# Kernel optimization log

Hardware: AMD Instinct MI355X
Metric: run time of the kernel (lower is better)

The kernel has to match this reference:

```python
import math
import jax, jax.numpy as jnp
import numpy as np

NUM_BUCKETS = 32
MAX_DISTANCE = 128
N_HEADS = 16
D_KV = 64


def relative_position_bucket(rel_pos, num_buckets=NUM_BUCKETS, max_distance=MAX_DISTANCE):
    # bidirectional=True path of the original
    n = -rel_pos
    nb = num_buckets // 2
    ret = (n < 0).astype(jnp.int32) * nb
    n = jnp.abs(n)
    max_exact = nb // 2
    is_small = n < max_exact
    val_large = max_exact + (
        jnp.log(n.astype(jnp.float32) / max_exact)
        / math.log(max_distance / max_exact)
        * (nb - max_exact)
    ).astype(jnp.int32)
    val_large = jnp.minimum(val_large, nb - 1)
    return jnp.where(is_small, n, val_large) + ret


def setup_inputs() -> dict:
    key = jax.random.key(0)
    ks = jax.random.split(key, 6)
    B, S, D = 2, 2048, 1024
    inner = N_HEADS * D_KV  # 1024
    sc = 1.0 / math.sqrt(D)
    return {
        "x": jax.random.normal(ks[0], (B, S, D), dtype=jnp.float32),
        "Wq": jax.random.normal(ks[1], (D, inner), dtype=jnp.float32) * sc,
        "Wk": jax.random.normal(ks[2], (D, inner), dtype=jnp.float32) * sc,
        "Wv": jax.random.normal(ks[3], (D, inner), dtype=jnp.float32) * sc,
        "Wo": jax.random.normal(ks[4], (inner, D), dtype=jnp.float32) * sc,
        "rel_table": jax.random.normal(ks[5], (NUM_BUCKETS, N_HEADS), dtype=jnp.float32),
        "attention_mask": jnp.zeros((B, 1, 1, S), dtype=jnp.float32),
    }


def reference(x, Wq, Wk, Wv, Wo, rel_table, attention_mask):
    B, S, D = x.shape
    H, Dk = N_HEADS, D_KV

    q = (x @ Wq).reshape(B, S, H, Dk).transpose(0, 2, 1, 3)  # bhqd
    k = (x @ Wk).reshape(B, S, H, Dk).transpose(0, 2, 1, 3)
    v = (x @ Wv).reshape(B, S, H, Dk).transpose(0, 2, 1, 3)

    # NOTE: T5 attention has no 1/sqrt(d) scaling
    scores = jnp.einsum('bhqd,bhkd->bhqk', q.astype(jnp.float32), k.astype(jnp.float32))

    pos = jnp.arange(S)
    rel_pos = pos[None, :] - pos[:, None]  # [S,S] = k_pos - q_pos
    buckets = relative_position_bucket(rel_pos)
    position_bias = jnp.transpose(rel_table[buckets], (2, 0, 1))  # [H,S,S]

    scores = scores + position_bias[None, ...] + attention_mask
    weights = jax.nn.softmax(scores, axis=-1)
    out = jnp.einsum('bhqk,bhkd->bhqd', weights, v.astype(jnp.float32))
    out = out.transpose(0, 2, 1, 3).reshape(B, S, H * Dk).astype(x.dtype)
    out = out @ Wo
    return (out, position_bias)
```

## Files before the change

kernel.cpp:

```cpp
#include <hip/hip_runtime.h>
#include <hip/hip_bf16.h>
#include <math.h>
#include <stdint.h>

typedef __bf16 bf16_t;
typedef __attribute__((ext_vector_type(8))) __bf16 bf16x8;
typedef __attribute__((ext_vector_type(4))) float f32x4;
typedef float f32x4a __attribute__((ext_vector_type(4), aligned(4)));
typedef unsigned short u16;
typedef unsigned int u32;

#define DEV static __device__ __forceinline__
#define LOG2E 1.4426950408889634f

DEV u16 f2b(float f){ bf16_t h = (bf16_t)f; return __builtin_bit_cast(u16, h); }
DEV float b2f(u16 u){ bf16_t h = __builtin_bit_cast(bf16_t, u); return (float)h; }
DEV f32x4 mfma16(bf16x8 a, bf16x8 b, f32x4 c){
  return __builtin_amdgcn_mfma_f32_16x16x32_bf16(a, b, c, 0, 0, 0);
}

#if __has_builtin(__builtin_amdgcn_exp2f)
DEV float fexp2(float x){ return __builtin_amdgcn_exp2f(x); }
#else
DEV float fexp2(float x){ return exp2f(x); }
#endif

DEV void gld16(const void* g, void* l){
  __builtin_amdgcn_global_load_lds((const __attribute__((address_space(1))) u32*)g,
                                   (__attribute__((address_space(3))) u32*)l, 16, 0, 0);
}

DEV bf16x8 ldsA64(const u16* arr, int row, int ch){
  return *(const bf16x8*)&arr[row*64 + ((ch ^ (row&7))*8)];
}
DEV bf16x8 ldsA32(const u16* arr, int row, int ch){
  return *(const bf16x8*)&arr[row*32 + ((ch ^ ((row>>1)&3))*8)];
}

__global__ __launch_bounds__(256) void k_prep(const float* __restrict__ x,
                                              const float* __restrict__ Wq, const float* __restrict__ Wk,
                                              const float* __restrict__ Wv, const float* __restrict__ Wo,
                                              const float* __restrict__ rel_table, const float* __restrict__ mask,
                                              u16* __restrict__ xh, u16* __restrict__ xl,
                                              u16* __restrict__ wth, u16* __restrict__ wot,
                                              float* __restrict__ bt, float* __restrict__ bt2,
                                              float* __restrict__ msk2){
  __shared__ float tile[64][65];
  int bid = blockIdx.x;
  int t = threadIdx.x;
  if(bid < 4096){
    size_t i = ((size_t)bid*256 + t)*4;
    float4 v = *(const float4*)(x + i);
    ushort4 hv, lv; float f, hf;
    f=v.x; hv.x=f2b(f); hf=b2f(hv.x); lv.x=f2b(f-hf);
    f=v.y; hv.y=f2b(f); hf=b2f(hv.y); lv.y=f2b(f-hf);
    f=v.z; hv.z=f2b(f); hf=b2f(hv.z); lv.z=f2b(f-hf);
    f=v.w; hv.w=f2b(f); hf=b2f(hv.w); lv.w=f2b(f-hf);
    *(ushort4*)(xh+i) = hv;
    *(ushort4*)(xl+i) = lv;
  } else if(bid < 5120){
    int rr = bid - 4096;
    int z = rr >> 8, ky = (rr >> 4) & 15, nx = rr & 15;
    const float* W = (z==0)?Wq:((z==1)?Wk:((z==2)?Wv:Wo));
    int n0 = nx*64, k0 = ky*64;
    int r = t>>6, c = t&63;
    #pragma unroll
    for(int i=0;i<16;i++){
      int row = i*4 + r;
      tile[row][c] = W[(size_t)(k0+row)*1024 + n0 + c];
    }
    __syncthreads();
    #pragma unroll
    for(int i=0;i<16;i++){
      int nrow = i*4 + r;
      float v = tile[c][nrow];
      size_t o = (size_t)(n0+nrow)*1024 + k0 + c;
      if(z<3) wth[(size_t)z*1048576 + o] = f2b(v);
      else    wot[o] = f2b(v);
    }
  } else {
    int gid = (bid-5120)*256 + t;
    if(gid < 4096) msk2[gid] = mask[gid]*LOG2E;
    int h = gid >> 12, idx = gid & 4095;
    float v = 0.f;
    if(idx < 4095){
      int delta = idx - 2047;
      int n = -delta;
      int ret = 0;
      if(n < 0){ ret = 16; n = -n; }
      int bucket;
      if(n < 8) bucket = n + ret;
      else {
        float a = (float)log((double)n * 0.125);
        float rr2 = (float)((double)a / (double)2.7725887298583984f);
        int vl = 8 + (int)(rr2 * 8.0f);
        vl = vl > 15 ? 15 : vl;
        bucket = vl + ret;
      }
      v = rel_table[bucket*16 + h];
    }
    bt[gid] = v;
    bt2[gid] = v*LOG2E - 32.0f;
  }
}

__global__ __launch_bounds__(256) void k_gemm_qkv(const u16* __restrict__ xh, const u16* __restrict__ xl,
                                                  const u16* __restrict__ wth,
                                                  u16* __restrict__ qh, u16* __restrict__ ql,
                                                  u16* __restrict__ kh, u16* __restrict__ vt){
  __shared__ __align__(16) u16 SM[24576];
  int z = blockIdx.z;
  const u16* WH = wth + (size_t)z*1048576;
  int lin2 = blockIdx.x + 8*blockIdx.y;
  int nl2 = (lin2 & 7)*32 + (lin2 >> 3);
  int n0 = (nl2 & 7)*128, m0 = (nl2 >> 3)*128;
  int t = threadIdx.x, w = t>>6, lane = t&63, l16 = lane&15, g = lane>>4;
  f32x4 acc[4][4];
  #pragma unroll
  for(int i=0;i<4;i++)
    #pragma unroll
    for(int j=0;j<4;j++) acc[i][j] = {0.f,0.f,0.f,0.f};
  int rbase = (w>>1)*64, cbase = (w&1)*64;

  #pragma unroll
  for(int jj=0;jj<6;jj++){
    int q = w + 4*jj;
    int arr = q>>3, sub = q&7;
    if(z!=0 && arr==1) continue;
    int row = sub*16 + (lane>>2);
    int lch = (lane&3) ^ ((row>>1)&3);
    const u16* src;
    if(arr==0)      src = xh + (size_t)(m0+row)*1024 + lch*8;
    else if(arr==1) src = xl + (size_t)(m0+row)*1024 + lch*8;
    else            src = WH + (size_t)(n0+row)*1024 + lch*8;
    gld16(src, &SM[q*512]);
  }
  __syncthreads();

  for(int it=0; it<32; ++it){
    const u16* Ah = SM + (it&1)*12288;
    const u16* Al = Ah + 4096;
    const u16* Bh = Ah + 8192;
    if(it < 31){
      u16* dstb = SM + ((it+1)&1)*12288;
      int kn = (it+1)*32;
      #pragma unroll
      for(int jj=0;jj<6;jj++){
        int q = w + 4*jj;
        int arr = q>>3, sub = q&7;
        if(z!=0 && arr==1) continue;
        int row = sub*16 + (lane>>2);
        int lch = (lane&3) ^ ((row>>1)&3);
        const u16* src;
        if(arr==0)      src = xh + (size_t)(m0+row)*1024 + kn + lch*8;
        else if(arr==1) src = xl + (size_t)(m0+row)*1024 + kn + lch*8;
        else            src = WH + (size_t)(n0+row)*1024 + kn + lch*8;
        gld16(src, dstb + q*512);
      }
      __builtin_amdgcn_sched_barrier(0);
    }
    if(z!=0){
      bf16x8 ah[4];
      #pragma unroll
      for(int i=0;i<4;i++) ah[i] = ldsA32(Ah, rbase + i*16 + l16, g);
      #pragma unroll
      for(int j=0;j<4;j++){
        bf16x8 bh = ldsA32(Bh, cbase + j*16 + l16, g);
        #pragma unroll
        for(int i=0;i<4;i++)
          acc[i][j] = mfma16(ah[i], bh, acc[i][j]);
      }
    } else {
      bf16x8 ah[4], am[4];
      #pragma unroll
      for(int i=0;i<4;i++){
        int row = rbase + i*16 + l16;
        ah[i] = ldsA32(Ah, row, g);
        am[i] = ldsA32(Al, row, g);
      }
      #pragma unroll
      for(int j=0;j<4;j++){
        bf16x8 bh = ldsA32(Bh, cbase + j*16 + l16, g);
        #pragma unroll
        for(int i=0;i<4;i++){
          acc[i][j] = mfma16(ah[i], bh, acc[i][j]);
          acc[i][j] = mfma16(am[i], bh, acc[i][j]);
        }
      }
    }
    __syncthreads();
  }
  if(z==2){
    #pragma unroll
    for(int i=0;i<4;i++)
      #pragma unroll
      for(int j=0;j<4;j++)
        #pragma unroll
        for(int r=0;r<4;r++){
          int ml = rbase + i*16 + g*4 + r;
          int nl = cbase + j*16 + l16;
          SM[nl*136 + ml] = f2b(acc[i][j][r]);
        }
    __syncthreads();
    int bb = m0 >> 11;
    #pragma unroll
    for(int kk=0;kk<8;kk++){
      int id = t + 256*kk;
      int row = id>>4, ch = id&15;
      uint4 v = *(const uint4*)&SM[row*136 + ch*8];
      int n = n0 + row;
      size_t dst = ((size_t)(bb*16 + (n>>6))*64 + (n&63))*2048 + (m0&2047) + ch*8;
      *(uint4*)&vt[dst] = v;
    }
  } else {
    #pragma unroll
    for(int i=0;i<4;i++)
      #pragma unroll
      for(int j=0;j<4;j++)
        #pragma unroll
        for(int r=0;r<4;r++){
          int m = m0 + rbase + i*16 + g*4 + r;
          int n = n0 + cbase + j*16 + l16;
          float v = acc[i][j][r];
          if(z==0) v *= LOG2E;
          int b = m >> 11, s = m & 2047;
          int hh = n >> 6, d = n & 63;
          size_t a = ((size_t)(b*16+hh)*2048 + s)*64 + d;
          u16 hb = f2b(v);
          if(z==0){ qh[a]=hb; ql[a]=f2b(v - b2f(hb)); }
          else    { kh[a]=hb; }
        }
  }
}

__global__ __launch_bounds__(256,4) void k_attn(const u16* __restrict__ qh, const u16* __restrict__ ql,
                                              const u16* __restrict__ kh,
                                              const u16* __restrict__ vt, const float* __restrict__ bt2,
                                              const float* __restrict__ msk2,
                                              const float* __restrict__ bt, float* __restrict__ bias_out,
                                              u16* __restrict__ ao){
  __shared__ __align__(16) u16 SM[20480];
  int lin = blockIdx.x + 32*blockIdx.y;
  int nlw = (lin & 7)*128 + (lin >> 3);
  int qx = nlw & 31, bh = nlw >> 5;
  int b = bh>>4, h = bh&15;
  int q0 = qx*64;
  int t = threadIdx.x, w = t>>6, lane = t&63, l16 = lane&15, g = lane>>4;
  int wr = w>>1, wc = w&1;
  size_t base  = (size_t)bh*2048*64;
  size_t vbase = (size_t)bh*64*2048;
  u16* PSq = SM + 16384 + w*1024;
  const float* bt2h = bt2 + h*4096;
  const float* msk2b = msk2 + b*2048;
  size_t wbase = ((size_t)(bh*32 + qx))*65536 + t*8;

  bf16x8 qfh[2][2], qfl[2][2];
  #pragma unroll
  for(int jq=0;jq<2;jq++){
    int qr = q0 + wr*32 + jq*16 + l16;
    size_t a0 = base + (size_t)qr*64 + g*8;
    qfh[jq][0] = *(const bf16x8*)&qh[a0];
    qfl[jq][0] = *(const bf16x8*)&ql[a0];
    qfh[jq][1] = *(const bf16x8*)&qh[a0+32];
    qfl[jq][1] = *(const bf16x8*)&ql[a0+32];
  }
  f32x4 O[2][4];
  float rsw[2] = {0.f, 0.f};
  #pragma unroll
  for(int jq=0;jq<2;jq++)
    #pragma unroll
    for(int jd=0;jd<4;jd++) O[jq][jd] = {0.f,0.f,0.f,0.f};

  #pragma unroll
  for(int jj=0;jj<4;jj++){
    int q = w + 4*jj;
    int arr = q>>3, sub = q&7;
    int row = sub*8 + (lane>>3);
    int lch = (lane&7) ^ (row&7);
    const u16* src = (arr==0) ? kh + base + (size_t)row*64 + lch*8
                              : vt + vbase + (size_t)row*2048 + lch*8;
    gld16(src, &SM[q*512]);
  }
  __syncthreads();

  for(int it=0; it<32; ++it){
    int k0 = it*64;
    const u16* KH = SM + (it&1)*8192;
    const u16* VT = KH + 4096;
    if(it < 31){
      u16* dstb = SM + ((it+1)&1)*8192;
      int kn = k0 + 64;
      #pragma unroll
      for(int jj=0;jj<4;jj++){
        int q = w + 4*jj;
        int arr = q>>3, sub = q&7;
        int row = sub*8 + (lane>>3);
        int lch = (lane&7) ^ (row&7);
        const u16* src = (arr==0) ? kh + base + (size_t)(kn+row)*64 + lch*8
                                  : vt + vbase + (size_t)row*2048 + kn + lch*8;
        gld16(src, dstb + q*512);
      }
      __builtin_amdgcn_sched_barrier(0);
    }
    {
      size_t f = wbase + (size_t)it*2048;
      int hh = (int)(f >> 22);
      int rem = (int)(f & 4194303);
      int qq = rem >> 11;
      int kk = rem & 2047;
      const float* row = bt + hh*4096 + (kk - qq + 2047);
      f32x4a v0 = *(const f32x4a*)(row);
      f32x4a v1 = *(const f32x4a*)(row + 4);
      __builtin_nontemporal_store(v0, (f32x4a*)(bias_out + f));
      __builtin_nontemporal_store(v1, (f32x4a*)(bias_out + f + 4));
    }
    f32x4 sc[2][2];
    {
      int kb = k0 + wc*32 + g*4;
      const float* mm = msk2b + kb;
      const float* bb = bt2h + (kb + 2047 - (q0 + wr*32 + l16));
      #pragma unroll
      for(int jq=0;jq<2;jq++)
        #pragma unroll
        for(int j=0;j<2;j++){
          f32x4a bvv = *(const f32x4a*)(bb + j*16 - jq*16);
          f32x4a mvv = *(const f32x4a*)(mm + j*16);
          sc[jq][j] = (f32x4){bvv[0]+mvv[0], bvv[1]+mvv[1], bvv[2]+mvv[2], bvv[3]+mvv[3]};
        }
    }
    __builtin_amdgcn_s_setprio(1);
    #pragma unroll
    for(int j=0;j<2;j++){
      int krow = wc*32 + j*16 + l16;
      bf16x8 kfh0 = ldsA64(KH, krow, g);
      bf16x8 kfh1 = ldsA64(KH, krow, 4+g);
      #pragma unroll
      for(int jq=0;jq<2;jq++){
        f32x4 s = sc[jq][j];
        s = mfma16(kfh0, qfh[jq][0], s);
        s = mfma16(kfh0, qfl[jq][0], s);
        s = mfma16(kfh1, qfh[jq][1], s);
        s = mfma16(kfh1, qfl[jq][1], s);
        sc[jq][j] = s;
      }
    }
    __builtin_amdgcn_s_setprio(0);
    #pragma unroll
    for(int jq=0;jq<2;jq++)
      #pragma unroll
      for(int j=0;j<2;j++){
        float p0 = fexp2(sc[jq][j][0]);
        float p1 = fexp2(sc[jq][j][1]);
        float p2 = fexp2(sc[jq][j][2]);
        float p3 = fexp2(sc[jq][j][3]);
        rsw[jq] += (p0+p1) + (p2+p3);
        ushort4 us = { f2b(p0), f2b(p1), f2b(p2), f2b(p3) };
        int rowp = jq*16 + l16;
        int c8 = j*2 + (g>>1);
        *(ushort4*)&PSq[rowp*32 + ((c8 ^ ((rowp>>1)&3))*8) + (g&1)*4] = us;
      }
    __builtin_amdgcn_s_setprio(1);
    {
      bf16x8 vbh[4];
      #pragma unroll
      for(int jd=0;jd<4;jd++) vbh[jd] = ldsA64(VT, jd*16 + l16, wc*4 + g);
      #pragma unroll
      for(int jq=0;jq<2;jq++){
        bf16x8 pa = ldsA32(PSq, jq*16 + l16, g);
        #pragma unroll
        for(int jd=0;jd<4;jd++)
          O[jq][jd] = mfma16(pa, vbh[jd], O[jq][jd]);
      }
    }
    __builtin_amdgcn_s_setprio(0);
    __syncthreads();
  }

  float* Of = (float*)SM;
  if(wc == 1){
    #pragma unroll
    for(int jq=0;jq<2;jq++)
      #pragma unroll
      for(int jd=0;jd<4;jd++){
        int c = jq*4 + jd;
        *(f32x4*)&Of[wr*2048 + lane*32 + ((c ^ (lane&7))*4)] = O[jq][jd];
      }
    float* rsf = (float*)&SM[16384 + w*1024];
    rsf[lane] = rsw[0];
    rsf[64+lane] = rsw[1];
  }
  __syncthreads();
  if(wc == 0){
    float* rsf = (float*)&SM[16384 + (w+1)*1024];
    float tot0 = rsw[0] + rsf[lane];
    float tot1 = rsw[1] + rsf[64+lane];
    tot0 += __shfl_xor(tot0, 16, 64);
    tot0 += __shfl_xor(tot0, 32, 64);
    tot1 += __shfl_xor(tot1, 16, 64);
    tot1 += __shfl_xor(tot1, 32, 64);
    #pragma unroll
    for(int jq=0;jq<2;jq++)
      #pragma unroll
      for(int jd=0;jd<4;jd++){
        int c = jq*4 + jd;
        f32x4 part = *(const f32x4*)&Of[wr*2048 + lane*32 + ((c ^ (lane&7))*4)];
        O[jq][jd] += part;
      }
    #pragma unroll
    for(int jq=0;jq<2;jq++){
      float tj = (jq==0) ? tot0 : tot1;
      #pragma unroll
      for(int r=0;r<4;r++){
        float inv = 1.f/__shfl(tj, g*4+r, 64);
        int q = q0 + wr*32 + jq*16 + g*4 + r;
        size_t a = ((size_t)(b*2048 + q))*1024 + h*64;
        #pragma unroll
        for(int jd=0;jd<4;jd++)
          ao[a + jd*16 + l16] = f2b(O[jq][jd][r]*inv);
      }
    }
  }
}

__global__ __launch_bounds__(256) void k_gemm_out(const u16* __restrict__ ao, const u16* __restrict__ wot,
                                                  float* __restrict__ out){
  __shared__ __align__(16) u16 SM[12288];
  int lin2 = blockIdx.x + 16*blockIdx.y;
  int nl2 = (lin2 & 7)*64 + (lin2 >> 3);
  int n0 = (nl2 & 15)*64, m0 = (nl2 >> 4)*128;
  int t = threadIdx.x, w = t>>6, lane = t&63, l16 = lane&15, g = lane>>4;
  f32x4 acc[4][2];
  #pragma unroll
  for(int i=0;i<4;i++)
    #pragma unroll
    for(int j=0;j<2;j++) acc[i][j] = {0.f,0.f,0.f,0.f};
  int rbase = (w>>1)*64, cbase = (w&1)*32;

  #pragma unroll
  for(int jj=0;jj<3;jj++){
    int q = w + 4*jj;
    int arr = q>>3, sub = q&7;
    int row = sub*16 + (lane>>2);
    int lch = (lane&3) ^ ((row>>1)&3);
    const u16* src = (arr==0) ? ao  + (size_t)(m0+row)*1024 + lch*8
                              : wot + (size_t)(n0+row)*1024 + lch*8;
    gld16(src, &SM[q*512]);
  }
  __syncthreads();

  for(int it=0; it<32; ++it){
    const u16* As = SM + (it&1)*6144;
    const u16* Bs = As + 4096;
    if(it < 31){
      u16* dstb = SM + ((it+1)&1)*6144;
      int kn = (it+1)*32;
      #pragma unroll
      for(int jj=0;jj<3;jj++){
        int q = w + 4*jj;
        int arr = q>>3, sub = q&7;
        int row = sub*16 + (lane>>2);
        int lch = (lane&3) ^ ((row>>1)&3);
        const u16* src = (arr==0) ? ao  + (size_t)(m0+row)*1024 + kn + lch*8
                                  : wot + (size_t)(n0+row)*1024 + kn + lch*8;
        gld16(src, dstb + q*512);
      }
      __builtin_amdgcn_sched_barrier(0);
    }
    bf16x8 af[4];
    #pragma unroll
    for(int i=0;i<4;i++) af[i] = ldsA32(As, rbase + i*16 + l16, g);
    #pragma unroll
    for(int j=0;j<2;j++){
      bf16x8 bfb = ldsA32(Bs, cbase + j*16 + l16, g);
      #pragma unroll
      for(int i=0;i<4;i++)
        acc[i][j] = mfma16(af[i], bfb, acc[i][j]);
    }
    __syncthreads();
  }
  #pragma unroll
  for(int i=0;i<4;i++)
    #pragma unroll
    for(int j=0;j<2;j++)
      #pragma unroll
      for(int r=0;r<4;r++){
        int m = m0 + rbase + i*16 + g*4 + r;
        int n = n0 + cbase + j*16 + l16;
        __builtin_nontemporal_store(acc[i][j][r], &out[(size_t)m*1024 + n]);
      }
}

extern "C" void kernel_launch(void* const* d_in, const int* in_sizes, int n_in,
                              void* d_out, int out_size, void* d_ws, size_t ws_size,
                              hipStream_t stream) {
  const float* x   = (const float*)d_in[0];
  const float* Wq  = (const float*)d_in[1];
  const float* Wk  = (const float*)d_in[2];
  const float* Wv  = (const float*)d_in[3];
  const float* Wo  = (const float*)d_in[4];
  const float* rel = (const float*)d_in[5];
  const float* msk = (const float*)d_in[6];
  float* out = (float*)d_out;
  float* bias_out = out + (size_t)4194304;
  char* ws = (char*)d_ws;
  u16* xh  = (u16*)(ws + 0);
  u16* xl  = (u16*)(ws + 8388608);
  u16* wth = (u16*)(ws + 16777216);
  u16* wot = (u16*)(ws + 23068672);
  u16* qh  = (u16*)(ws + 25165824);
  u16* ql  = (u16*)(ws + 33554432);
  u16* kh  = (u16*)(ws + 41943040);
  u16* vt  = (u16*)(ws + 50331648);
  u16* ao  = (u16*)(ws + 58720256);
  float* bt  = (float*)(ws + 67108864);
  float* bt2 = (float*)(ws + 67371008);
  float* msk2= (float*)(ws + 67633152);

  k_prep      <<<5376, 256, 0, stream>>>(x, Wq, Wk, Wv, Wo, rel, msk,
                                         xh, xl, wth, wot, bt, bt2, msk2);
  k_gemm_qkv  <<<dim3(8,32,3), 256, 0, stream>>>(xh, xl, wth, qh, ql, kh, vt);
  k_attn      <<<dim3(32,32), 256, 0, stream>>>(qh, ql, kh, vt, bt2, msk2, bt, bias_out, ao);
  k_gemm_out  <<<dim3(16,32), 256, 0, stream>>>(ao, wot, out);
}
```

Measured before the change: 454.3 us.

## Split Q projection into narrower tiles and specialize K/V GEMM paths

The QKV projection grid gains a fourth z-slice. The Q projection, which needs twice the MFMAs because it uses hi/lo split precision, is now done in 128x64 tiles across two slices, while K and V use a dedicated single-precision path with smaller shared memory. This evens out per-block work and removes runtime z-branches inside the inner loop. It also lowers the k_attn launch-bounds occupancy hint from 4 to 3 blocks, giving the compiler more registers per thread at the cost of fewer resident blocks.

```diff
diff --git a/kernel.cpp b/kernel.cpp
--- a/kernel.cpp
+++ b/kernel.cpp
@@ -108,69 +108,59 @@
                                                   const u16* __restrict__ wth,
                                                   u16* __restrict__ qh, u16* __restrict__ ql,
                                                   u16* __restrict__ kh, u16* __restrict__ vt){
-  __shared__ __align__(16) u16 SM[24576];
-  int z = blockIdx.z;
-  const u16* WH = wth + (size_t)z*1048576;
+  __shared__ __align__(16) u16 SM[20480];
+  int zp = blockIdx.z;
   int lin2 = blockIdx.x + 8*blockIdx.y;
   int nl2 = (lin2 & 7)*32 + (lin2 >> 3);
-  int n0 = (nl2 & 7)*128, m0 = (nl2 >> 3)*128;
+  int m0 = (nl2 >> 3)*128;
   int t = threadIdx.x, w = t>>6, lane = t&63, l16 = lane&15, g = lane>>4;
-  f32x4 acc[4][4];
-  #pragma unroll
-  for(int i=0;i<4;i++)
-    #pragma unroll
-    for(int j=0;j<4;j++) acc[i][j] = {0.f,0.f,0.f,0.f};
-  int rbase = (w>>1)*64, cbase = (w&1)*64;
-
-  #pragma unroll
-  for(int jj=0;jj<6;jj++){
-    int q = w + 4*jj;
-    int arr = q>>3, sub = q&7;
-    if(z!=0 && arr==1) continue;
-    int row = sub*16 + (lane>>2);
-    int lch = (lane&3) ^ ((row>>1)&3);
-    const u16* src;
-    if(arr==0)      src = xh + (size_t)(m0+row)*1024 + lch*8;
-    else if(arr==1) src = xl + (size_t)(m0+row)*1024 + lch*8;
-    else            src = WH + (size_t)(n0+row)*1024 + lch*8;
-    gld16(src, &SM[q*512]);
-  }
-  __syncthreads();
-
-  for(int it=0; it<32; ++it){
-    const u16* Ah = SM + (it&1)*12288;
-    const u16* Al = Ah + 4096;
-    const u16* Bh = Ah + 8192;
-    if(it < 31){
-      u16* dstb = SM + ((it+1)&1)*12288;
-      int kn = (it+1)*32;
-      #pragma unroll
-      for(int jj=0;jj<6;jj++){
-        int q = w + 4*jj;
-        int arr = q>>3, sub = q&7;
-        if(z!=0 && arr==1) continue;
-        int row = sub*16 + (lane>>2);
-        int lch = (lane&3) ^ ((row>>1)&3);
-        const u16* src;
-        if(arr==0)      src = xh + (size_t)(m0+row)*1024 + kn + lch*8;
-        else if(arr==1) src = xl + (size_t)(m0+row)*1024 + kn + lch*8;
-        else            src = WH + (size_t)(n0+row)*1024 + kn + lch*8;
-        gld16(src, dstb + q*512);
-      }
-      __builtin_amdgcn_sched_barrier(0);
-    }
-    if(z!=0){
-      bf16x8 ah[4];
-      #pragma unroll
-      for(int i=0;i<4;i++) ah[i] = ldsA32(Ah, rbase + i*16 + l16, g);
-      #pragma unroll
-      for(int j=0;j<4;j++){
-        bf16x8 bh = ldsA32(Bh, cbase + j*16 + l16, g);
-        #pragma unroll
-        for(int i=0;i<4;i++)
-          acc[i][j] = mfma16(ah[i], bh, acc[i][j]);
-      }
-    } else {
+  int rbase = (w>>1)*64;
+
+  if(zp < 2){
+    int n0 = zp*512 + (nl2 & 7)*64;
+    const u16* WH = wth;
+    int cbase = (w&1)*32;
+    f32x4 acc[4][2];
+    #pragma unroll
+    for(int i=0;i<4;i++)
+      #pragma unroll
+      for(int j=0;j<2;j++) acc[i][j] = {0.f,0.f,0.f,0.f};
+
+    #pragma unroll
+    for(int jj=0;jj<5;jj++){
+      int q = w + 4*jj;
+      int arr = q>>3, sub = q&7;
+      int row = sub*16 + (lane>>2);
+      int lch = (lane&3) ^ ((row>>1)&3);
+      const u16* src;
+      if(arr==0)      src = xh + (size_t)(m0+row)*1024 + lch*8;
+      else if(arr==1) src = xl + (size_t)(m0+row)*1024 + lch*8;
+      else            src = WH + (size_t)(n0+row)*1024 + lch*8;
+      gld16(src, &SM[q*512]);
+    }
+    __syncthreads();
+
+    for(int it=0; it<32; ++it){
+      const u16* Ah = SM + (it&1)*10240;
+      const u16* Al = Ah + 4096;
+      const u16* Bh = Ah + 8192;
+      if(it < 31){
+        u16* dstb = SM + ((it+1)&1)*10240;
+        int kn = (it+1)*32;
+        #pragma unroll
+        for(int jj=0;jj<5;jj++){
+          int q = w + 4*jj;
+          int arr = q>>3, sub = q&7;
+          int row = sub*16 + (lane>>2);
+          int lch = (lane&3) ^ ((row>>1)&3);
+          const u16* src;
+          if(arr==0)      src = xh + (size_t)(m0+row)*1024 + kn + lch*8;
+          else if(arr==1) src = xl + (size_t)(m0+row)*1024 + kn + lch*8;
+          else            src = WH + (size_t)(n0+row)*1024 + kn + lch*8;
+          gld16(src, dstb + q*512);
+        }
+        __builtin_amdgcn_sched_barrier(0);
+      }
       bf16x8 ah[4], am[4];
       #pragma unroll
       for(int i=0;i<4;i++){
@@ -179,7 +169,7 @@
         am[i] = ldsA32(Al, row, g);
       }
       #pragma unroll
-      for(int j=0;j<4;j++){
+      for(int j=0;j<2;j++){
         bf16x8 bh = ldsA32(Bh, cbase + j*16 + l16, g);
         #pragma unroll
         for(int i=0;i<4;i++){
@@ -187,53 +177,118 @@
           acc[i][j] = mfma16(am[i], bh, acc[i][j]);
         }
       }
-    }
-    __syncthreads();
-  }
-  if(z==2){
+      __syncthreads();
+    }
     #pragma unroll
     for(int i=0;i<4;i++)
       #pragma unroll
-      for(int j=0;j<4;j++)
-        #pragma unroll
-        for(int r=0;r<4;r++){
-          int ml = rbase + i*16 + g*4 + r;
-          int nl = cbase + j*16 + l16;
-          SM[nl*136 + ml] = f2b(acc[i][j][r]);
-        }
-    __syncthreads();
-    int bb = m0 >> 11;
-    #pragma unroll
-    for(int kk=0;kk<8;kk++){
-      int id = t + 256*kk;
-      int row = id>>4, ch = id&15;
-      uint4 v = *(const uint4*)&SM[row*136 + ch*8];
-      int n = n0 + row;
-      size_t dst = ((size_t)(bb*16 + (n>>6))*64 + (n&63))*2048 + (m0&2047) + ch*8;
-      *(uint4*)&vt[dst] = v;
-    }
-  } else {
-    #pragma unroll
-    for(int i=0;i<4;i++)
-      #pragma unroll
-      for(int j=0;j<4;j++)
+      for(int j=0;j<2;j++)
         #pragma unroll
         for(int r=0;r<4;r++){
           int m = m0 + rbase + i*16 + g*4 + r;
           int n = n0 + cbase + j*16 + l16;
-          float v = acc[i][j][r];
-          if(z==0) v *= LOG2E;
+          float v = acc[i][j][r] * LOG2E;
           int b = m >> 11, s = m & 2047;
           int hh = n >> 6, d = n & 63;
           size_t a = ((size_t)(b*16+hh)*2048 + s)*64 + d;
           u16 hb = f2b(v);
-          if(z==0){ qh[a]=hb; ql[a]=f2b(v - b2f(hb)); }
-          else    { kh[a]=hb; }
+          qh[a] = hb;
+          ql[a] = f2b(v - b2f(hb));
         }
-  }
-}
-
-__global__ __launch_bounds__(256,4) void k_attn(const u16* __restrict__ qh, const u16* __restrict__ ql,
+  } else {
+    int z = zp - 1;
+    int n0 = (nl2 & 7)*128;
+    const u16* WH = wth + (size_t)z*1048576;
+    int cbase = (w&1)*64;
+    f32x4 acc[4][4];
+    #pragma unroll
+    for(int i=0;i<4;i++)
+      #pragma unroll
+      for(int j=0;j<4;j++) acc[i][j] = {0.f,0.f,0.f,0.f};
+
+    #pragma unroll
+    for(int jj=0;jj<4;jj++){
+      int q = w + 4*jj;
+      int arr = q>>3, sub = q&7;
+      int row = sub*16 + (lane>>2);
+      int lch = (lane&3) ^ ((row>>1)&3);
+      const u16* src = (arr==0) ? xh + (size_t)(m0+row)*1024 + lch*8
+                                : WH + (size_t)(n0+row)*1024 + lch*8;
+      gld16(src, &SM[q*512]);
+    }
+    __syncthreads();
+
+    for(int it=0; it<32; ++it){
+      const u16* As = SM + (it&1)*8192;
+      const u16* Bs = As + 4096;
+      if(it < 31){
+        u16* dstb = SM + ((it+1)&1)*8192;
+        int kn = (it+1)*32;
+        #pragma unroll
+        for(int jj=0;jj<4;jj++){
+          int q = w + 4*jj;
+          int arr = q>>3, sub = q&7;
+          int row = sub*16 + (lane>>2);
+          int lch = (lane&3) ^ ((row>>1)&3);
+          const u16* src = (arr==0) ? xh + (size_t)(m0+row)*1024 + kn + lch*8
+                                    : WH + (size_t)(n0+row)*1024 + kn + lch*8;
+          gld16(src, dstb + q*512);
+        }
+        __builtin_amdgcn_sched_barrier(0);
+      }
+      bf16x8 ah[4];
+      #pragma unroll
+      for(int i=0;i<4;i++) ah[i] = ldsA32(As, rbase + i*16 + l16, g);
+      #pragma unroll
+      for(int j=0;j<4;j++){
+        bf16x8 bh = ldsA32(Bs, cbase + j*16 + l16, g);
+        #pragma unroll
+        for(int i=0;i<4;i++)
+          acc[i][j] = mfma16(ah[i], bh, acc[i][j]);
+      }
+      __syncthreads();
+    }
+    if(z==2){
+      #pragma unroll
+      for(int i=0;i<4;i++)
+        #pragma unroll
+        for(int j=0;j<4;j++)
+          #pragma unroll
+          for(int r=0;r<4;r++){
+            int ml = rbase + i*16 + g*4 + r;
+            int nl = cbase + j*16 + l16;
+            SM[nl*136 + ml] = f2b(acc[i][j][r]);
+          }
+      __syncthreads();
+      int bb = m0 >> 11;
+      #pragma unroll
+      for(int kk=0;kk<8;kk++){
+        int id = t + 256*kk;
+        int row = id>>4, ch = id&15;
+        uint4 v = *(const uint4*)&SM[row*136 + ch*8];
+        int n = n0 + row;
+        size_t dst = ((size_t)(bb*16 + (n>>6))*64 + (n&63))*2048 + (m0&2047) + ch*8;
+        *(uint4*)&vt[dst] = v;
+      }
+    } else {
+      #pragma unroll
+      for(int i=0;i<4;i++)
+        #pragma unroll
+        for(int j=0;j<4;j++)
+          #pragma unroll
+          for(int r=0;r<4;r++){
+            int m = m0 + rbase + i*16 + g*4 + r;
+            int n = n0 + cbase + j*16 + l16;
+            int b = m >> 11, s = m & 2047;
+            int hh = n >> 6, d = n & 63;
+            size_t a = ((size_t)(b*16+hh)*2048 + s)*64 + d;
+            kh[a] = f2b(acc[i][j][r]);
+          }
+    }
+  }
+}
+
+__global__ __launch_bounds__(256,3) void k_attn(const u16* __restrict__ qh, const u16* __restrict__ ql,
                                               const u16* __restrict__ kh,
                                               const u16* __restrict__ vt, const float* __restrict__ bt2,
                                               const float* __restrict__ msk2,
@@ -518,7 +573,7 @@
 
   k_prep      <<<5376, 256, 0, stream>>>(x, Wq, Wk, Wv, Wo, rel, msk,
                                          xh, xl, wth, wot, bt, bt2, msk2);
-  k_gemm_qkv  <<<dim3(8,32,3), 256, 0, stream>>>(xh, xl, wth, qh, ql, kh, vt);
+  k_gemm_qkv  <<<dim3(8,32,4), 256, 0, stream>>>(xh, xl, wth, qh, ql, kh, vt);
   k_attn      <<<dim3(32,32), 256, 0, stream>>>(qh, ql, kh, vt, bt2, msk2, bt, bias_out, ao);
   k_gemm_out  <<<dim3(16,32), 256, 0, stream>>>(ao, wot, out);
 }
```

Measured after the change: 439.7 us. 3.2% less time.
